# Kernel optimization log

Hardware: AMD Instinct MI355X
Metric: run time of the kernel (lower is better)

Reference implementation:

```python
import jax, jax.numpy as jnp
import numpy as np


def setup_inputs() -> dict:
    key = jax.random.key(0)
    k1, k2, k3 = jax.random.split(key, 3)
    B, C, Z, S, T, H = 8, 128, 4, 8, 1024, 64
    WQ = jax.random.normal(k1, (C, Z, S, H), dtype=jnp.float32)
    WK = jax.random.normal(k2, (B, Z, T, H), dtype=jnp.float32)
    K = jax.random.normal(k3, (B, Z, T, H), dtype=jnp.float32)
    return {"WQ": WQ, "WK": WK, "K": K}


def reference(WQ, WK, K):
    # tanh non-linearities on keys (WQ is used raw, as in the original)
    WKt = jnp.tanh(WK)          # [b,z,t,h]
    Kt = jnp.tanh(K)            # [b,z,t,h]
    # attention scores per (batch, code, group, synonym) over tokens t
    scores = jnp.einsum('bzth,czsh->bczst', WKt, WQ)   # [b,c,z,s,t]
    attn = jax.nn.softmax(scores, axis=-1)             # softmax over t
    # weighted sum of (tanh'd) values over tokens
    context = jnp.einsum('bzth,bczst->bczsh', Kt, attn)  # [b,c,z,s,h]
    # AvgPool3d((1, s, 1)) then squeeze(-2) == mean over synonym axis s
    context = jnp.mean(context, axis=3)                  # [b,c,z,h]
    return (scores, context, attn)
```

## Files before the change

kernel.cpp:

```cpp
#include <hip/hip_runtime.h>

typedef _Float16 f16;
typedef f16 f16x4 __attribute__((ext_vector_type(4)));
typedef f16 f16x8 __attribute__((ext_vector_type(8)));
typedef float f32x16 __attribute__((ext_vector_type(16)));

#define NB 8
#define NC 128
#define NZ 4
#define NS 8
#define NT 1024
#define NH 64

#define WQ_N (NC*NZ*NS*NH)
#define WK_N (NB*NZ*NT*NH)

#define OUT_CTX  (NB*NC*NZ*NS*NT)
#define OUT_ATTN (OUT_CTX + NB*NC*NZ*NH)

__global__ __launch_bounds__(256) void prep_kernel(
    const float* __restrict__ WQ, const float* __restrict__ WK, const float* __restrict__ K,
    f16* __restrict__ wqh, f16* __restrict__ wkh, f16* __restrict__ ktT)
{
    __shared__ f16 ldsT[64*64];
    const int tid = threadIdx.x;
    const int blk = blockIdx.x;
    if (blk < 512) {
        const int bz = blk >> 4;
        const int t0 = (blk & 15) << 6;
        #pragma unroll
        for (int it = 0; it < 4; ++it) {
            int idx = it*256 + tid;
            int tl  = idx >> 4;
            int seg = idx & 15;
            int gi  = (bz*NT + t0 + tl)*NH + seg*4;
            float4 wk4 = *(const float4*)(WK + gi);
            float4 k4  = *(const float4*)(K  + gi);
            f16x4 wv;
            wv[0] = (f16)tanhf(wk4.x);
            wv[1] = (f16)tanhf(wk4.y);
            wv[2] = (f16)tanhf(wk4.z);
            wv[3] = (f16)tanhf(wk4.w);
            *(f16x4*)(wkh + gi) = wv;
            ldsT[(seg*4+0)*64 + tl] = (f16)tanhf(k4.x);
            ldsT[(seg*4+1)*64 + tl] = (f16)tanhf(k4.y);
            ldsT[(seg*4+2)*64 + tl] = (f16)tanhf(k4.z);
            ldsT[(seg*4+3)*64 + tl] = (f16)tanhf(k4.w);
        }
        __syncthreads();
        #pragma unroll
        for (int it = 0; it < 4; ++it) {
            int idx = it*256 + tid;
            int h  = idx >> 4;
            int ts = idx & 15;
            f16x4 v = *(const f16x4*)&ldsT[h*64 + ts*4];
            *(f16x4*)(ktT + (bz*NH + h)*NT + t0 + ts*4) = v;
        }
    } else {
        const int ib = blk - 512;
        #pragma unroll
        for (int it = 0; it < 16; ++it) {
            int gi = ib*16384 + it*1024 + tid*4;
            float4 q = *(const float4*)(WQ + gi);
            f16x4 w;
            w[0] = (f16)q.x; w[1] = (f16)q.y; w[2] = (f16)q.z; w[3] = (f16)q.w;
            *(f16x4*)(wqh + gi) = w;
        }
    }
}

__global__ __launch_bounds__(256, 2) void fused_kernel(
    const f16* __restrict__ wqh, const f16* __restrict__ wkh, const f16* __restrict__ ktT,
    float* __restrict__ scores, float* __restrict__ attn, float* __restrict__ ctxout)
{
    __shared__ float rsL[4][32];
    __shared__ float invL[32];
    __shared__ f16   attnB[4][1024];
    __shared__ float ctxW[4][32][64];

    const int tid  = threadIdx.x;
    const int wave = tid >> 6;
    const int lane = tid & 63;
    const int l31  = lane & 31;
    const int g    = lane >> 5;
    const int bid  = blockIdx.x;
    const int bz = bid & 31, mt = bid >> 5;
    const int b = bz >> 2, z = bz & 3;
    const int m0 = mt * 32;

    const int mgA = m0 + l31;
    const f16* ap = wqh + (((mgA >> 3)*NZ + z)*NS + (mgA & 7))*NH + g*8;
    f16x8 afr[4];
    #pragma unroll
    for (int st = 0; st < 4; ++st) afr[st] = *(const f16x8*)(ap + st*16);

    f32x16 acc[8];
    #pragma unroll
    for (int tt = 0; tt < 8; ++tt)
        #pragma unroll
        for (int r = 0; r < 16; ++r) acc[tt][r] = 0.f;

    #pragma unroll
    for (int tt = 0; tt < 8; ++tt) {
        const int t0 = (tt*4 + wave) * 32;
        const f16* bp = wkh + (bz*NT + t0 + l31)*NH + g*8;
        #pragma unroll
        for (int st = 0; st < 4; ++st) {
            f16x8 bfr = *(const f16x8*)(bp + st*16);
            acc[tt] = __builtin_amdgcn_mfma_f32_32x32x16_f16(afr[st], bfr, acc[tt], 0, 0, 0);
        }
    }

    const int base2 = ((b*NC + mt*4)*NZ + z)*NS*NT;
    float p[16];
    #pragma unroll
    for (int r = 0; r < 16; ++r) p[r] = 0.f;

    #pragma unroll
    for (int tt = 0; tt < 8; ++tt) {
        const int tcol = (tt*4 + wave)*32 + l31;
        #pragma unroll
        for (int r = 0; r < 16; ++r) {
            int off = base2 + (r >> 2)*32768 + ((r & 3) + 4*g)*1024 + tcol;
            float v = acc[tt][r];
            scores[off] = v;
            float e = __expf(v);
            acc[tt][r] = e;
            p[r] += e;
        }
    }

    #pragma unroll
    for (int d = 1; d < 32; d <<= 1)
        #pragma unroll
        for (int r = 0; r < 16; ++r) p[r] += __shfl_xor(p[r], d, 64);

    if (l31 == 0) {
        #pragma unroll
        for (int r = 0; r < 16; ++r) rsL[wave][(r & 3) + 8*(r >> 2) + 4*g] = p[r];
    }
    __syncthreads();
    if (tid < 32) invL[tid] = 1.0f / (rsL[0][tid] + rsL[1][tid] + rsL[2][tid] + rsL[3][tid]);
    __syncthreads();

    f32x16 cacc[2];
    #pragma unroll
    for (int nt = 0; nt < 2; ++nt)
        #pragma unroll
        for (int r = 0; r < 16; ++r) cacc[nt][r] = 0.f;

    #pragma unroll
    for (int tt = 0; tt < 8; ++tt) {
        const int t0 = (tt*4 + wave) * 32;
        const int tcol = t0 + l31;
        #pragma unroll
        for (int r = 0; r < 16; ++r) {
            int ml = (r & 3) + 8*(r >> 2) + 4*g;
            float a = acc[tt][r] * invL[ml];
            int off = base2 + (r >> 2)*32768 + ((r & 3) + 4*g)*1024 + tcol;
            attn[off] = a;
            int tb = l31 >> 3;
            int ai = ((tb*32 + ml)*8 + (l31 & 7)) ^ (tb << 3);
            attnB[wave][ai] = (f16)a;
        }
        #pragma unroll
        for (int s2 = 0; s2 < 2; ++s2) {
            int tb = 2*s2 + g;
            int ai = ((tb*32 + l31)*8) ^ (tb << 3);
            f16x8 pa = *(const f16x8*)&attnB[wave][ai];
            #pragma unroll
            for (int nt = 0; nt < 2; ++nt) {
                const f16* bp2 = ktT + (bz*NH + nt*32 + l31)*NT + t0 + s2*16 + g*8;
                f16x8 bf = *(const f16x8*)bp2;
                cacc[nt] = __builtin_amdgcn_mfma_f32_32x32x16_f16(pa, bf, cacc[nt], 0, 0, 0);
            }
        }
    }

    #pragma unroll
    for (int nt = 0; nt < 2; ++nt) {
        #pragma unroll
        for (int r = 0; r < 16; ++r) {
            int ml = (r & 3) + 8*(r >> 2) + 4*g;
            ctxW[wave][ml][nt*32 + l31] = cacc[nt][r];
        }
    }
    __syncthreads();

    {
        int cl = tid >> 6;
        int h  = tid & 63;
        float sum = 0.f;
        #pragma unroll
        for (int w = 0; w < 4; ++w)
            #pragma unroll
            for (int q = 0; q < 8; ++q)
                sum += ctxW[w][cl*8 + q][h];
        ctxout[((b*NC + (m0 >> 3) + cl)*NZ + z)*NH + h] = sum * 0.125f;
    }
}

extern "C" void kernel_launch(void* const* d_in, const int* in_sizes, int n_in,
                              void* d_out, int out_size, void* d_ws, size_t ws_size,
                              hipStream_t stream)
{
    const float* WQ = (const float*)d_in[0];
    const float* WK = (const float*)d_in[1];
    const float* K  = (const float*)d_in[2];

    char* ws = (char*)d_ws;
    f16* wqh = (f16*)(ws);
    f16* wkh = (f16*)(ws + (size_t)WQ_N*2);
    f16* ktT = (f16*)(ws + (size_t)WQ_N*2 + (size_t)WK_N*2);

    float* out    = (float*)d_out;
    float* scores = out;
    float* ctxout = out + OUT_CTX;
    float* attn   = out + OUT_ATTN;

    hipLaunchKernelGGL(prep_kernel, dim3(528), dim3(256), 0, stream,
                       WQ, WK, K, wqh, wkh, ktT);
    hipLaunchKernelGGL(fused_kernel, dim3(1024), dim3(256), 0, stream,
                       wqh, wkh, ktT, scores, attn, ctxout);
}
```

Measured before the change: 71.86 us.

## Recompute score MFMAs in second pass to cut registers and raise occupancy

Drops the 8 held score accumulators. Scores are now recomputed with MFMA in the attn/context pass instead of kept in registers, which allows launch bounds to rise from 2 to 3 blocks per SIMD. Score and attn stores become nontemporal, and tanh in the prep kernel is replaced by an exp/rcp approximation. The trade-off is twice the score MFMA work plus reloading WK, and slightly lower tanh accuracy.

```diff
diff --git a/kernel.cpp b/kernel.cpp
--- a/kernel.cpp
+++ b/kernel.cpp
@@ -17,6 +17,11 @@
 
 #define OUT_CTX  (NB*NC*NZ*NS*NT)
 #define OUT_ATTN (OUT_CTX + NB*NC*NZ*NH)
+
+__device__ __forceinline__ float fast_tanh(float x) {
+    float e = __expf(2.0f * x);
+    return 1.0f - 2.0f * __builtin_amdgcn_rcpf(e + 1.0f);
+}
 
 __global__ __launch_bounds__(256) void prep_kernel(
     const float* __restrict__ WQ, const float* __restrict__ WK, const float* __restrict__ K,
@@ -37,15 +42,15 @@
             float4 wk4 = *(const float4*)(WK + gi);
             float4 k4  = *(const float4*)(K  + gi);
             f16x4 wv;
-            wv[0] = (f16)tanhf(wk4.x);
-            wv[1] = (f16)tanhf(wk4.y);
-            wv[2] = (f16)tanhf(wk4.z);
-            wv[3] = (f16)tanhf(wk4.w);
+            wv[0] = (f16)fast_tanh(wk4.x);
+            wv[1] = (f16)fast_tanh(wk4.y);
+            wv[2] = (f16)fast_tanh(wk4.z);
+            wv[3] = (f16)fast_tanh(wk4.w);
             *(f16x4*)(wkh + gi) = wv;
-            ldsT[(seg*4+0)*64 + tl] = (f16)tanhf(k4.x);
-            ldsT[(seg*4+1)*64 + tl] = (f16)tanhf(k4.y);
-            ldsT[(seg*4+2)*64 + tl] = (f16)tanhf(k4.z);
-            ldsT[(seg*4+3)*64 + tl] = (f16)tanhf(k4.w);
+            ldsT[(seg*4+0)*64 + tl] = (f16)fast_tanh(k4.x);
+            ldsT[(seg*4+1)*64 + tl] = (f16)fast_tanh(k4.y);
+            ldsT[(seg*4+2)*64 + tl] = (f16)fast_tanh(k4.z);
+            ldsT[(seg*4+3)*64 + tl] = (f16)fast_tanh(k4.w);
         }
         __syncthreads();
         #pragma unroll
@@ -69,7 +74,7 @@
     }
 }
 
-__global__ __launch_bounds__(256, 2) void fused_kernel(
+__global__ __launch_bounds__(256, 3) void fused_kernel(
     const f16* __restrict__ wqh, const f16* __restrict__ wkh, const f16* __restrict__ ktT,
     float* __restrict__ scores, float* __restrict__ attn, float* __restrict__ ctxout)
 {
@@ -94,39 +99,30 @@
     #pragma unroll
     for (int st = 0; st < 4; ++st) afr[st] = *(const f16x8*)(ap + st*16);
 
-    f32x16 acc[8];
-    #pragma unroll
-    for (int tt = 0; tt < 8; ++tt)
-        #pragma unroll
-        for (int r = 0; r < 16; ++r) acc[tt][r] = 0.f;
-
-    #pragma unroll
+    const int base2 = ((b*NC + mt*4)*NZ + z)*NS*NT;
+
+    float p[16];
+    #pragma unroll
+    for (int r = 0; r < 16; ++r) p[r] = 0.f;
+
+    #pragma unroll 2
     for (int tt = 0; tt < 8; ++tt) {
         const int t0 = (tt*4 + wave) * 32;
         const f16* bp = wkh + (bz*NT + t0 + l31)*NH + g*8;
+        f32x16 acc;
+        #pragma unroll
+        for (int r = 0; r < 16; ++r) acc[r] = 0.f;
         #pragma unroll
         for (int st = 0; st < 4; ++st) {
             f16x8 bfr = *(const f16x8*)(bp + st*16);
-            acc[tt] = __builtin_amdgcn_mfma_f32_32x32x16_f16(afr[st], bfr, acc[tt], 0, 0, 0);
-        }
-    }
-
-    const int base2 = ((b*NC + mt*4)*NZ + z)*NS*NT;
-    float p[16];
-    #pragma unroll
-    for (int r = 0; r < 16; ++r) p[r] = 0.f;
-
-    #pragma unroll
-    for (int tt = 0; tt < 8; ++tt) {
-        const int tcol = (tt*4 + wave)*32 + l31;
+            acc = __builtin_amdgcn_mfma_f32_32x32x16_f16(afr[st], bfr, acc, 0, 0, 0);
+        }
+        const int tcol = t0 + l31;
         #pragma unroll
         for (int r = 0; r < 16; ++r) {
-            int off = base2 + (r >> 2)*32768 + ((r & 3) + 4*g)*1024 + tcol;
-            float v = acc[tt][r];
-            scores[off] = v;
-            float e = __expf(v);
-            acc[tt][r] = e;
-            p[r] += e;
+            float v = acc[r];
+            __builtin_nontemporal_store(v, scores + base2 + (r >> 2)*32768 + ((r & 3) + 4*g)*1024 + tcol);
+            p[r] += __expf(v);
         }
     }
 
@@ -149,16 +145,24 @@
         #pragma unroll
         for (int r = 0; r < 16; ++r) cacc[nt][r] = 0.f;
 
-    #pragma unroll
+    #pragma unroll 2
     for (int tt = 0; tt < 8; ++tt) {
         const int t0 = (tt*4 + wave) * 32;
+        const f16* bp = wkh + (bz*NT + t0 + l31)*NH + g*8;
+        f32x16 acc;
+        #pragma unroll
+        for (int r = 0; r < 16; ++r) acc[r] = 0.f;
+        #pragma unroll
+        for (int st = 0; st < 4; ++st) {
+            f16x8 bfr = *(const f16x8*)(bp + st*16);
+            acc = __builtin_amdgcn_mfma_f32_32x32x16_f16(afr[st], bfr, acc, 0, 0, 0);
+        }
         const int tcol = t0 + l31;
         #pragma unroll
         for (int r = 0; r < 16; ++r) {
             int ml = (r & 3) + 8*(r >> 2) + 4*g;
-            float a = acc[tt][r] * invL[ml];
-            int off = base2 + (r >> 2)*32768 + ((r & 3) + 4*g)*1024 + tcol;
-            attn[off] = a;
+            float a = __expf(acc[r]) * invL[ml];
+            __builtin_nontemporal_store(a, attn + base2 + (r >> 2)*32768 + ((r & 3) + 4*g)*1024 + tcol);
             int tb = l31 >> 3;
             int ai = ((tb*32 + ml)*8 + (l31 & 7)) ^ (tb << 3);
             attnB[wave][ai] = (f16)a;
```

Result: slower. 81.30 us (+13.1%).
